# Kernel optimization log

Hardware: AMD Instinct MI355X
Metric: run time of the kernel (lower is better)

The kernel has to match this reference:

```python
import jax, jax.numpy as jnp
import numpy as np

B, L, N, C = 64, 12, 4096, 3
FD, HD, OUT = 32, 64, 12
TID, DIW, TD = 288, 7, 16
STEPS = 4
EMB = 10  # node embedding dim for learned adjacency


def setup_inputs() -> dict:
    key = jax.random.key(0)
    ks = jax.random.split(key, 16)
    g = lambda i, shape, s=0.05: jax.random.normal(ks[i], shape, dtype=jnp.float32) * s
    z = lambda n: jnp.zeros((n,), jnp.float32)
    return {
        "history_data": jax.random.uniform(ks[0], (B, L, N, C), dtype=jnp.float32),
        "future_data": jnp.zeros((B, L, N, 1), jnp.float32),
        "batch_seen": 0,
        "epoch": 0,
        "train": 1,
        "tid_emb": g(1, (TID, TD)),
        "diw_emb": g(2, (DIW, TD)),
        "t2f_w": g(3, (2 * TD, FD)), "t2f_b": z(FD),
        "enc_w1": g(4, (L * C, HD)), "enc_b1": z(HD),
        "enc_w2": g(5, (HD, FD)), "enc_b2": z(FD),
        "node_emb": g(6, (N, EMB), 1.0),
        "pde_w1": g(7, (FD, HD)), "pde_b1": z(HD),
        "pde_w2": g(8, (HD, FD)), "pde_b2": z(FD),
        "ss_win": g(9, (FD, FD)), "ss_wst": g(10, (FD, FD)), "ss_b": z(FD),
        "ss_wout": g(11, (FD, FD)), "ss_bout": z(FD),
        "dec_w1": g(12, (FD, HD)), "dec_b1": z(HD),
        "dec_w2": g(13, (HD, OUT)), "dec_b2": z(OUT),
        "pde_mix": jnp.array(0.5, jnp.float32),
    }


def reference(history_data, future_data, batch_seen, epoch, train,
              tid_emb, diw_emb, t2f_w, t2f_b,
              enc_w1, enc_b1, enc_w2, enc_b2,
              node_emb,
              pde_w1, pde_b1, pde_w2, pde_b2,
              ss_win, ss_wst, ss_b, ss_wout, ss_bout,
              dec_w1, dec_b1, dec_w2, dec_b2, pde_mix):
    # --- encoder: per-node MLP over flattened (L, C) history ---
    x = history_data[..., :C]                                    # [B,L,N,C]
    x = jnp.transpose(x, (0, 2, 1, 3)).reshape(B, N, L * C)      # [B,N,L*C]
    field = jnp.maximum(x @ enc_w1 + enc_b1, 0.0) @ enc_w2 + enc_b2  # [B,N,FD]

    # --- temporal field bias from last-step tid/diw ---
    tid_idx = jnp.clip((history_data[:, -1, :, 1] * TID).astype(jnp.int32), 0, TID - 1)
    diw_idx = jnp.clip((history_data[:, -1, :, 2] * DIW).astype(jnp.int32), 0, DIW - 1)
    temp = jnp.concatenate([tid_emb[tid_idx], diw_emb[diw_idx]], axis=-1)  # [B,N,2*TD]
    field = field + temp @ t2f_w + t2f_b

    # --- learned adjacency for graph Laplacian (L = I - A) ---
    A = jax.nn.softmax(jnp.maximum(node_emb @ node_emb.T, 0.0), axis=-1)  # [N,N]

    alpha = jax.nn.sigmoid(pde_mix)
    dt = 1.0 / STEPS
    state = jnp.zeros_like(field)
    for _ in range(STEPS):  # fixed small unroll over PDE steps
        L_F = jnp.einsum('nm,bmf->bnf', A, field) - field         # (A - I) F
        N_F = jnp.maximum(field @ pde_w1 + pde_b1, 0.0) @ pde_w2 + pde_b2
        fe = field + (alpha * L_F + (1.0 - alpha) * N_F) * dt
        state = jnp.tanh(fe @ ss_win + state @ ss_wst + ss_b)     # state-space update
        field = fe + state @ ss_wout + ss_bout

    # --- decoder: per-node MLP to output horizon ---
    pred = jnp.maximum(field @ dec_w1 + dec_b1, 0.0) @ dec_w2 + dec_b2  # [B,N,OUT]
    return jnp.transpose(pred, (0, 2, 1))[..., None]              # [B,OUT,N,1]
```

## Files before the change

kernel.cpp:

```cpp
#include <hip/hip_runtime.h>

#define BATCH 64
#define LHIST 12
#define NNODE 4096
#define CCH   3
#define FD    32
#define HD    64
#define OUTD  12
#define TIDN  288
#define DIWN  7
#define TDD   16
#define EMBD  10
#define MROWS 2048
#define KDIM  4096
#define MTOT  (BATCH * NNODE)

typedef __attribute__((ext_vector_type(8))) short bf16x8;
typedef __attribute__((ext_vector_type(4))) float f32x4;

union BF8U { bf16x8 v; unsigned short s[8]; };

__device__ __forceinline__ unsigned short f2b(float f) {
    union { float f; unsigned u; } v; v.f = f;
    unsigned r = v.u + 0x7fffu + ((v.u >> 16) & 1u);
    return (unsigned short)(r >> 16);
}

__device__ __forceinline__ float b2f(unsigned short u) {
    union { unsigned u; float f; } v; v.u = (unsigned)u << 16; return v.f;
}

__device__ __forceinline__ float fast_tanh(float x) {
    x = fminf(fmaxf(x, -15.f), 15.f);
    const float e = __expf(2.f * x);
    return (e - 1.f) / (e + 1.f);
}

__device__ __forceinline__ bf16x8 ldsfrag(const unsigned short* p) {
    return *(const bf16x8*)p;
}

__device__ __forceinline__ bf16x8 pack8(float4 a, float4 b) {
    BF8U u;
    u.s[0] = f2b(a.x); u.s[1] = f2b(a.y); u.s[2] = f2b(a.z); u.s[3] = f2b(a.w);
    u.s[4] = f2b(b.x); u.s[5] = f2b(b.y); u.s[6] = f2b(b.z); u.s[7] = f2b(b.w);
    return u.v;
}

__global__ __launch_bounds__(256) void build_A(const float* __restrict__ emb,
                                               unsigned short* __restrict__ A) {
    const int n = blockIdx.x;
    const int tid = threadIdx.x;
    __shared__ float sc[NNODE];
    __shared__ float red[256];
    float e[EMBD];
#pragma unroll
    for (int c = 0; c < EMBD; c++) e[c] = emb[(size_t)n * EMBD + c];
    float mx = 0.f;
    for (int m = tid; m < NNODE; m += 256) {
        float s = 0.f;
#pragma unroll
        for (int c = 0; c < EMBD; c++) s += e[c] * emb[(size_t)m * EMBD + c];
        s = fmaxf(s, 0.f);
        sc[m] = s;
        mx = fmaxf(mx, s);
    }
    red[tid] = mx;
    __syncthreads();
    for (int off = 128; off > 0; off >>= 1) {
        if (tid < off) red[tid] = fmaxf(red[tid], red[tid + off]);
        __syncthreads();
    }
    mx = red[0];
    __syncthreads();
    float sum = 0.f;
    for (int m = tid; m < NNODE; m += 256) {
        float v = expf(sc[m] - mx);
        sc[m] = v;
        sum += v;
    }
    red[tid] = sum;
    __syncthreads();
    for (int off = 128; off > 0; off >>= 1) {
        if (tid < off) red[tid] += red[tid + off];
        __syncthreads();
    }
    const float inv = 1.f / red[0];
    for (int m = tid; m < NNODE; m += 256)
        A[(size_t)n * NNODE + m] = f2b(sc[m] * inv);
}

__global__ __launch_bounds__(256, 2) void encoder(const float* __restrict__ hist,
                                                  const float* __restrict__ tid_emb,
                                                  const float* __restrict__ diw_emb,
                                                  const float* __restrict__ t2f_w,
                                                  const float* __restrict__ t2f_b,
                                                  const float* __restrict__ enc_w1,
                                                  const float* __restrict__ enc_b1,
                                                  const float* __restrict__ enc_w2,
                                                  const float* __restrict__ enc_b2,
                                                  float* __restrict__ field,
                                                  unsigned short* __restrict__ fT) {
    const int gid = blockIdx.x * 256 + threadIdx.x;
    const int b = gid >> 12;
    const int n = gid & (NNODE - 1);
    const float* hb = hist + ((size_t)b * LHIST * NNODE + n) * CCH;
    float x[LHIST * CCH];
#pragma unroll
    for (int l = 0; l < LHIST; l++) {
        x[l * 3 + 0] = hb[(size_t)l * NNODE * CCH + 0];
        x[l * 3 + 1] = hb[(size_t)l * NNODE * CCH + 1];
        x[l * 3 + 2] = hb[(size_t)l * NNODE * CCH + 2];
    }
    float f[FD];
#pragma unroll
    for (int o = 0; o < FD; o++) f[o] = enc_b2[o] + t2f_b[o];
    for (int j = 0; j < HD; j++) {
        float h = enc_b1[j];
#pragma unroll
        for (int k = 0; k < LHIST * CCH; k++) h += x[k] * enc_w1[k * HD + j];
        h = fmaxf(h, 0.f);
#pragma unroll
        for (int o = 0; o < FD; o++) f[o] += h * enc_w2[j * FD + o];
    }
    const int ti = min(max((int)(x[11 * 3 + 1] * 288.0f), 0), TIDN - 1);
    const int di = min(max((int)(x[11 * 3 + 2] * 7.0f), 0), DIWN - 1);
    for (int g = 0; g < TDD; g++) {
        const float tg = tid_emb[ti * TDD + g];
        const float dg = diw_emb[di * TDD + g];
#pragma unroll
        for (int o = 0; o < FD; o++)
            f[o] += tg * t2f_w[g * FD + o] + dg * t2f_w[(TDD + g) * FD + o];
    }
#pragma unroll
    for (int o4 = 0; o4 < FD / 4; o4++) {
        float4 v = {f[o4 * 4 + 0], f[o4 * 4 + 1], f[o4 * 4 + 2], f[o4 * 4 + 3]};
        *(float4*)&field[(size_t)gid * FD + o4 * 4] = v;
    }
#pragma unroll
    for (int o = 0; o < FD; o++)
        fT[(size_t)(b * FD + o) * NNODE + n] = f2b(f[o]);
}

#define TPAD 36
#define QHP  72
#define QFP  40
__global__ __launch_bounds__(256) void gemm_step(const unsigned short* __restrict__ X,
                                                 const unsigned short* __restrict__ Y,
                                                 float* __restrict__ field,
                                                 unsigned short* __restrict__ state,
                                                 unsigned short* __restrict__ fTo,
                                                 const float* __restrict__ pde_w1,
                                                 const float* __restrict__ pde_b1,
                                                 const float* __restrict__ pde_w2,
                                                 const float* __restrict__ pde_b2,
                                                 const float* __restrict__ ss_win,
                                                 const float* __restrict__ ss_wst,
                                                 const float* __restrict__ ss_b,
                                                 const float* __restrict__ ss_wout,
                                                 const float* __restrict__ ss_bout,
                                                 const float* __restrict__ pde_mix,
                                                 int first) {
    constexpr int K = KDIM;
    constexpr int BK = 32;
    __shared__ __align__(16) unsigned short SM0[512 * TPAD];
    __shared__ __align__(16) unsigned short W1T[HD * FD];
    __shared__ __align__(16) unsigned short W2T[FD * HD];
    __shared__ __align__(16) unsigned short WinT[FD * FD];
    __shared__ __align__(16) unsigned short WstT[FD * FD];
    __shared__ __align__(16) unsigned short WoutT[FD * FD];
    __shared__ __align__(16) unsigned short Hs[4 * 32 * QHP];
    __shared__ __align__(16) unsigned short Fs[4 * 32 * QFP];

    const int tid = threadIdx.x;
    const int wave = tid >> 6;
    const int lane = tid & 63;

    for (int i = tid; i < HD * FD; i += 256) W1T[(i & 63) * FD + (i >> 6)] = f2b(pde_w1[i]);
    for (int i = tid; i < HD * FD; i += 256) W2T[(i & 31) * HD + (i >> 5)] = f2b(pde_w2[i]);
    for (int i = tid; i < FD * FD; i += 256) {
        WinT [(i & 31) * FD + (i >> 5)] = f2b(ss_win[i]);
        WstT [(i & 31) * FD + (i >> 5)] = f2b(ss_wst[i]);
        WoutT[(i & 31) * FD + (i >> 5)] = f2b(ss_wout[i]);
    }

    const int l = blockIdx.x + 16 * blockIdx.y;
    const int xcd = l & 7;
    const int rem = l >> 3;
    const int by = xcd * 4 + (rem & 3);
    const int bx = rem >> 2;
    const int i0 = bx * 128;
    const int j0 = by * 128;
    const int b0 = i0 >> 5;

    const int wi = (wave >> 1) * 64;
    const int wj = (wave & 1) * 64;

    const int lrow = lane >> 2;
    const int gcol = (lane & 3) * 8;
    const int scol = ((lane & 3) ^ ((lane >> 3) & 3)) * 8;

    const unsigned short* Xg = X + (size_t)(i0 + wave * 32 + lrow) * K + gcol;
    const unsigned short* Yg = Y + (size_t)(j0 + wave * 32 + lrow) * K + gcol;
    unsigned short* Xs = SM0;
    unsigned short* Ys = SM0 + 8192;
    const int ld0 = (wave * 32 + lrow) * BK + scol;
    const int ld1 = (wave * 32 + 16 + lrow) * BK + scol;

    const f32x4 zero = {0.f, 0.f, 0.f, 0.f};
    f32x4 acc[4][4];
#pragma unroll
    for (int a = 0; a < 4; a++)
#pragma unroll
        for (int b = 0; b < 4; b++) acc[a][b] = zero;

    const int fr = lane & 15;
    const int q = lane >> 4;
    const int kq8 = (q ^ ((fr >> 1) & 3)) * 8;

#define GS_COMPUTE(P)                                                              \
    {                                                                              \
        bf16x8 fa[4], fb[4];                                                       \
        _Pragma("unroll") for (int t = 0; t < 4; t++)                              \
            fa[t] = *(const bf16x8*)&Xs[(P) * 4096 + (wi + t * 16 + fr) * BK + kq8]; \
        _Pragma("unroll") for (int t = 0; t < 4; t++)                              \
            fb[t] = *(const bf16x8*)&Ys[(P) * 4096 + (wj + t * 16 + fr) * BK + kq8]; \
        _Pragma("unroll") for (int mi = 0; mi < 4; mi++)                           \
            _Pragma("unroll") for (int ni = 0; ni < 4; ni++)                       \
                acc[mi][ni] = __builtin_amdgcn_mfma_f32_16x16x32_bf16(             \
                    fa[mi], fb[ni], acc[mi][ni], 0, 0, 0);                         \
    }

    uint4 ax0 = *(const uint4*)(Xg);
    uint4 ax1 = *(const uint4*)(Xg + 16 * K);
    uint4 ay0 = *(const uint4*)(Yg);
    uint4 ay1 = *(const uint4*)(Yg + 16 * K);
    uint4 bx0 = *(const uint4*)(Xg + BK);
    uint4 bx1 = *(const uint4*)(Xg + BK + 16 * K);
    uint4 by0 = *(const uint4*)(Yg + BK);
    uint4 by1 = *(const uint4*)(Yg + BK + 16 * K);
    *(uint4*)&Xs[ld0] = ax0; *(uint4*)&Xs[ld1] = ax1;
    *(uint4*)&Ys[ld0] = ay0; *(uint4*)&Ys[ld1] = ay1;
    __syncthreads();

    int p = 0;
    for (int kt = 0; kt < K; kt += 2 * BK) {
        if (kt + 2 * BK < K) {
            ax0 = *(const uint4*)(Xg + kt + 2 * BK);
            ax1 = *(const uint4*)(Xg + kt + 2 * BK + 16 * K);
            ay0 = *(const uint4*)(Yg + kt + 2 * BK);
            ay1 = *(const uint4*)(Yg + kt + 2 * BK + 16 * K);
        }
        GS_COMPUTE(p);
        {
            const int np = p ^ 1;
            *(uint4*)&Xs[np * 4096 + ld0] = bx0; *(uint4*)&Xs[np * 4096 + ld1] = bx1;
            *(uint4*)&Ys[np * 4096 + ld0] = by0; *(uint4*)&Ys[np * 4096 + ld1] = by1;
            __syncthreads();
        }
        if (kt + 3 * BK < K) {
            bx0 = *(const uint4*)(Xg + kt + 3 * BK);
            bx1 = *(const uint4*)(Xg + kt + 3 * BK + 16 * K);
            by0 = *(const uint4*)(Yg + kt + 3 * BK);
            by1 = *(const uint4*)(Yg + kt + 3 * BK + 16 * K);
        }
        GS_COMPUTE(p ^ 1);
        if (kt + 2 * BK < K) {
            *(uint4*)&Xs[p * 4096 + ld0] = ax0; *(uint4*)&Xs[p * 4096 + ld1] = ax1;
            *(uint4*)&Ys[p * 4096 + ld0] = ay0; *(uint4*)&Ys[p * 4096 + ld1] = ay1;
            __syncthreads();
        }
    }
#undef GS_COMPUTE

    __syncthreads();
    unsigned short* T = SM0;
    const int r0 = q * 4;
#pragma unroll
    for (int mi = 0; mi < 4; mi++) {
#pragma unroll
        for (int ni = 0; ni < 4; ni++) {
            const int R0 = i0 + wi + mi * 16 + r0;
            const int nl = wj + ni * 16 + fr;
            ushort4 pk = {f2b(acc[mi][ni][0]), f2b(acc[mi][ni][1]),
                          f2b(acc[mi][ni][2]), f2b(acc[mi][ni][3])};
            *(ushort4*)&T[((((R0 >> 5) & 3) << 7) + nl) * TPAD + (R0 & 31)] = pk;
        }
    }
    __syncthreads();

    const int ln = fr;
    const int kq = q * 8;
    unsigned short* Hw = &Hs[wave * 32 * QHP];
    unsigned short* Fw = &Fs[wave * 32 * QFP];
    const float alpha = 1.f / (1.f + __expf(-pde_mix[0]));
    const float dt = 0.25f;

    bf16x8 w1f[4], w2f[2][2], winf[2], wstf[2], woutf[2];
#pragma unroll
    for (int nj = 0; nj < 4; nj++) w1f[nj] = ldsfrag(&W1T[(nj * 16 + ln) * FD + kq]);
#pragma unroll
    for (int nf = 0; nf < 2; nf++) {
#pragma unroll
        for (int kk = 0; kk < 2; kk++)
            w2f[nf][kk] = ldsfrag(&W2T[(nf * 16 + ln) * HD + kk * 32 + kq]);
        winf[nf]  = ldsfrag(&WinT [(nf * 16 + ln) * FD + kq]);
        wstf[nf]  = ldsfrag(&WstT [(nf * 16 + ln) * FD + kq]);
        woutf[nf] = ldsfrag(&WoutT[(nf * 16 + ln) * FD + kq]);
    }
    float b1v[4], b2v[2], bsv[2], bov[2];
#pragma unroll
    for (int nj = 0; nj < 4; nj++) b1v[nj] = pde_b1[nj * 16 + ln];
#pragma unroll
    for (int nf = 0; nf < 2; nf++) {
        b2v[nf] = pde_b2[nf * 16 + ln];
        bsv[nf] = ss_b[nf * 16 + ln];
        bov[nf] = ss_bout[nf * 16 + ln];
    }

    for (int qtr = 0; qtr < 4; qtr++) {
        const int lb = wave * 128 + qtr * 32;
        const int bb = lb >> 7;
        const int nl0 = lb & 127;
        const int bg = b0 + bb;
        const int mwg = (bg << 12) + j0 + nl0;

        bf16x8 fA[2], stA[2];
#pragma unroll
        for (int mi = 0; mi < 2; mi++) {
            const float4* fp = (const float4*)&field[(size_t)(mwg + mi * 16 + ln) * FD + kq];
            fA[mi] = pack8(fp[0], fp[1]);
        }
        if (!first) {
#pragma unroll
            for (int mi = 0; mi < 2; mi++)
                stA[mi] = *(const bf16x8*)&state[(size_t)(mwg + mi * 16 + ln) * FD + kq];
        }

        f32x4 hc[2][4];
#pragma unroll
        for (int mi = 0; mi < 2; mi++)
#pragma unroll
            for (int nj = 0; nj < 4; nj++)
                hc[mi][nj] = __builtin_amdgcn_mfma_f32_16x16x32_bf16(fA[mi], w1f[nj], zero, 0, 0, 0);
#pragma unroll
        for (int mi = 0; mi < 2; mi++)
#pragma unroll
            for (int nj = 0; nj < 4; nj++)
#pragma unroll
                for (int r = 0; r < 4; r++)
                    Hw[(mi * 16 + r0 + r) * QHP + nj * 16 + ln] =
                        f2b(fmaxf(hc[mi][nj][r] + b1v[nj], 0.f));

        float fld[2][2][4], ctv[2][2][4];
#pragma unroll
        for (int mi = 0; mi < 2; mi++)
#pragma unroll
            for (int nf = 0; nf < 2; nf++)
#pragma unroll
                for (int r = 0; r < 4; r++) {
                    const size_t idx = (size_t)(mwg + mi * 16 + r0 + r) * FD + nf * 16 + ln;
                    fld[mi][nf][r] = field[idx];
                    ctv[mi][nf][r] = b2f(T[(lb + mi * 16 + r0 + r) * TPAD + nf * 16 + ln]);
                }

        bf16x8 hA[2][2];
#pragma unroll
        for (int mi = 0; mi < 2; mi++)
#pragma unroll
            for (int kk = 0; kk < 2; kk++)
                hA[mi][kk] = ldsfrag(&Hw[(mi * 16 + ln) * QHP + kk * 32 + kq]);
        f32x4 nc[2][2];
#pragma unroll
        for (int mi = 0; mi < 2; mi++)
#pragma unroll
            for (int nf = 0; nf < 2; nf++) {
                f32x4 a = __builtin_amdgcn_mfma_f32_16x16x32_bf16(hA[mi][0], w2f[nf][0], zero, 0, 0, 0);
                nc[mi][nf] = __builtin_amdgcn_mfma_f32_16x16x32_bf16(hA[mi][1], w2f[nf][1], a, 0, 0, 0);
            }

        float fe[2][2][4];
#pragma unroll
        for (int mi = 0; mi < 2; mi++)
#pragma unroll
            for (int nf = 0; nf < 2; nf++)
#pragma unroll
                for (int r = 0; r < 4; r++) {
                    const float nfv = nc[mi][nf][r] + b2v[nf];
                    const float fv = fld[mi][nf][r];
                    fe[mi][nf][r] = fv + (alpha * (ctv[mi][nf][r] - fv) + (1.f - alpha) * nfv) * dt;
                    Fw[(mi * 16 + r0 + r) * QFP + nf * 16 + ln] = f2b(fe[mi][nf][r]);
                }

        bf16x8 feA[2];
#pragma unroll
        for (int mi = 0; mi < 2; mi++) feA[mi] = ldsfrag(&Fw[(mi * 16 + ln) * QFP + kq]);
        f32x4 sc_[2][2];
#pragma unroll
        for (int mi = 0; mi < 2; mi++)
#pragma unroll
            for (int nf = 0; nf < 2; nf++) {
                f32x4 a = __builtin_amdgcn_mfma_f32_16x16x32_bf16(feA[mi], winf[nf], zero, 0, 0, 0);
                if (!first)
                    a = __builtin_amdgcn_mfma_f32_16x16x32_bf16(stA[mi], wstf[nf], a, 0, 0, 0);
                sc_[mi][nf] = a;
            }
        float sval[2][2][4];
#pragma unroll
        for (int mi = 0; mi < 2; mi++)
#pragma unroll
            for (int nf = 0; nf < 2; nf++)
#pragma unroll
                for (int r = 0; r < 4; r++)
                    sval[mi][nf][r] = fast_tanh(sc_[mi][nf][r] + bsv[nf]);
#pragma unroll
        for (int mi = 0; mi < 2; mi++)
#pragma unroll
            for (int nf = 0; nf < 2; nf++)
#pragma unroll
                for (int r = 0; r < 4; r++)
                    Fw[(mi * 16 + r0 + r) * QFP + nf * 16 + ln] = f2b(sval[mi][nf][r]);

        bf16x8 SA[2];
#pragma unroll
        for (int mi = 0; mi < 2; mi++) SA[mi] = ldsfrag(&Fw[(mi * 16 + ln) * QFP + kq]);
#pragma unroll
        for (int mi = 0; mi < 2; mi++) {
#pragma unroll
            for (int nf = 0; nf < 2; nf++) {
                f32x4 oc = __builtin_amdgcn_mfma_f32_16x16x32_bf16(SA[mi], woutf[nf], zero, 0, 0, 0);
                float fnew[4];
#pragma unroll
                for (int r = 0; r < 4; r++) {
                    fnew[r] = fe[mi][nf][r] + oc[r] + bov[nf];
                    const size_t idx = (size_t)(mwg + mi * 16 + r0 + r) * FD + nf * 16 + ln;
                    field[idx] = fnew[r];
                    state[idx] = f2b(sval[mi][nf][r]);
                }
                ushort4 pk = {f2b(fnew[0]), f2b(fnew[1]), f2b(fnew[2]), f2b(fnew[3])};
                const size_t fta = (size_t)(bg * FD + nf * 16 + ln) * NNODE
                                 + j0 + nl0 + mi * 16 + r0;
                *(ushort4*)&fTo[fta] = pk;
            }
        }
    }
}

__global__ __launch_bounds__(256) void gemm_bt(const unsigned short* __restrict__ X,
                                               const unsigned short* __restrict__ Y,
                                               unsigned short* __restrict__ Cp) {
    constexpr int K = KDIM;
    constexpr int KS = KDIM / 2;
    constexpr int BK = 32;
    __shared__ __align__(16) unsigned short Xs[2 * 4096];
    __shared__ __align__(16) unsigned short Ys[2 * 4096];
    const int tid = threadIdx.x;
    const int wave = tid >> 6;
    const int lane = tid & 63;

    const int l = blockIdx.x + 16 * blockIdx.y;
    const int xcd = l & 7;
    const int rem = l >> 3;
    const int by = xcd * 4 + (rem & 3);
    const int bx = rem >> 2;
    const int i0 = bx * 128;
    const int j0 = by * 128;
    const int k0 = blockIdx.z * KS;
    unsigned short* C = Cp + (size_t)blockIdx.z * MTOT * FD;

    const int wi = (wave >> 1) * 64;
    const int wj = (wave & 1) * 64;

    const int lrow = lane >> 2;
    const int gcol = (lane & 3) * 8;
    const int scol = ((lane & 3) ^ ((lane >> 3) & 3)) * 8;

    const unsigned short* Xg = X + (size_t)(i0 + wave * 32 + lrow) * K + k0 + gcol;
    const unsigned short* Yg = Y + (size_t)(j0 + wave * 32 + lrow) * K + k0 + gcol;
    const int ld0 = (wave * 32 + lrow) * BK + scol;
    const int ld1 = (wave * 32 + 16 + lrow) * BK + scol;

    const f32x4 zero = {0.f, 0.f, 0.f, 0.f};
    f32x4 acc[4][4];
#pragma unroll
    for (int a = 0; a < 4; a++)
#pragma unroll
        for (int b = 0; b < 4; b++) acc[a][b] = zero;

    const int fr = lane & 15;
    const int q = lane >> 4;
    const int kq8 = (q ^ ((fr >> 1) & 3)) * 8;

#define GB_COMPUTE(P)                                                              \
    {                                                                              \
        bf16x8 fa[4], fb[4];                                                       \
        _Pragma("unroll") for (int t = 0; t < 4; t++)                              \
            fa[t] = *(const bf16x8*)&Xs[(P) * 4096 + (wi + t * 16 + fr) * BK + kq8]; \
        _Pragma("unroll") for (int t = 0; t < 4; t++)                              \
            fb[t] = *(const bf16x8*)&Ys[(P) * 4096 + (wj + t * 16 + fr) * BK + kq8]; \
        _Pragma("unroll") for (int mi = 0; mi < 4; mi++)                           \
            _Pragma("unroll") for (int ni = 0; ni < 4; ni++)                       \
                acc[mi][ni] = __builtin_amdgcn_mfma_f32_16x16x32_bf16(             \
                    fa[mi], fb[ni], acc[mi][ni], 0, 0, 0);                         \
    }

    uint4 ax0 = *(const uint4*)(Xg);
    uint4 ax1 = *(const uint4*)(Xg + 16 * K);
    uint4 ay0 = *(const uint4*)(Yg);
    uint4 ay1 = *(const uint4*)(Yg + 16 * K);
    uint4 bx0 = *(const uint4*)(Xg + BK);
    uint4 bx1 = *(const uint4*)(Xg + BK + 16 * K);
    uint4 by0 = *(const uint4*)(Yg + BK);
    uint4 by1 = *(const uint4*)(Yg + BK + 16 * K);
    *(uint4*)&Xs[ld0] = ax0; *(uint4*)&Xs[ld1] = ax1;
    *(uint4*)&Ys[ld0] = ay0; *(uint4*)&Ys[ld1] = ay1;
    __syncthreads();

    int p = 0;
    for (int kt = 0; kt < KS; kt += 2 * BK) {
        if (kt + 2 * BK < KS) {
            ax0 = *(const uint4*)(Xg + kt + 2 * BK);
            ax1 = *(const uint4*)(Xg + kt + 2 * BK + 16 * K);
            ay0 = *(const uint4*)(Yg + kt + 2 * BK);
            ay1 = *(const uint4*)(Yg + kt + 2 * BK + 16 * K);
        }
        GB_COMPUTE(p);
        {
            const int np = p ^ 1;
            *(uint4*)&Xs[np * 4096 + ld0] = bx0; *(uint4*)&Xs[np * 4096 + ld1] = bx1;
            *(uint4*)&Ys[np * 4096 + ld0] = by0; *(uint4*)&Ys[np * 4096 + ld1] = by1;
            __syncthreads();
        }
        if (kt + 3 * BK < KS) {
            bx0 = *(const uint4*)(Xg + kt + 3 * BK);
            bx1 = *(const uint4*)(Xg + kt + 3 * BK + 16 * K);
            by0 = *(const uint4*)(Yg + kt + 3 * BK);
            by1 = *(const uint4*)(Yg + kt + 3 * BK + 16 * K);
        }
        GB_COMPUTE(p ^ 1);
        if (kt + 2 * BK < KS) {
            *(uint4*)&Xs[p * 4096 + ld0] = ax0; *(uint4*)&Xs[p * 4096 + ld1] = ax1;
            *(uint4*)&Ys[p * 4096 + ld0] = ay0; *(uint4*)&Ys[p * 4096 + ld1] = ay1;
            __syncthreads();
        }
    }
#undef GB_COMPUTE

    const int r0 = q * 4;
#pragma unroll
    for (int mi = 0; mi < 4; mi++) {
#pragma unroll
        for (int ni = 0; ni < 4; ni++) {
            const int R0 = i0 + wi + mi * 16 + r0;
            const int col = j0 + wj + ni * 16 + fr;
            const size_t addr = ((size_t)(R0 >> 5) * NNODE + col) * FD + (R0 & 31);
            ushort4 pk = {f2b(acc[mi][ni][0]), f2b(acc[mi][ni][1]),
                          f2b(acc[mi][ni][2]), f2b(acc[mi][ni][3])};
            *(ushort4*)&C[addr] = pk;
        }
    }
}

#define HPAD 72
#define FPAD 40
__global__ __launch_bounds__(256, 2) void step_mfma(const unsigned short* __restrict__ Ct0,
                                                    const unsigned short* __restrict__ Ct1,
                                                    float* __restrict__ field,
                                                    unsigned short* __restrict__ state,
                                                    const float* __restrict__ pde_w1,
                                                    const float* __restrict__ pde_b1,
                                                    const float* __restrict__ pde_w2,
                                                    const float* __restrict__ pde_b2,
                                                    const float* __restrict__ ss_win,
                                                    const float* __restrict__ ss_wst,
                                                    const float* __restrict__ ss_b,
                                                    const float* __restrict__ ss_wout,
                                                    const float* __restrict__ ss_bout,
                                                    const float* __restrict__ pde_mix,
                                                    const float* __restrict__ dec_w1,
                                                    const float* __restrict__ dec_b1,
                                                    const float* __restrict__ dec_w2,
                                                    const float* __restrict__ dec_b2,
                                                    float* __restrict__ out) {
    __shared__ __align__(16) unsigned short W1T[HD * FD];
    __shared__ __align__(16) unsigned short W2T[FD * HD];
    __shared__ __align__(16) unsigned short WinT[FD * FD];
    __shared__ __align__(16) unsigned short WstT[FD * FD];
    __shared__ __align__(16) unsigned short WoutT[FD * FD];
    __shared__ __align__(16) unsigned short Wd1T[HD * FD];
    __shared__ __align__(16) unsigned short Wd2T[16 * HD];
    __shared__ __align__(16) unsigned short Hs[4 * 64 * HPAD];
    __shared__ __align__(16) unsigned short Fs[4 * 64 * FPAD];

    const int tid = threadIdx.x;
    for (int i = tid; i < HD * FD; i += 256) W1T[(i & 63) * FD + (i >> 6)] = f2b(pde_w1[i]);
    for (int i = tid; i < HD * FD; i += 256) W2T[(i & 31) * HD + (i >> 5)] = f2b(pde_w2[i]);
    for (int i = tid; i < FD * FD; i += 256) {
        WinT [(i & 31) * FD + (i >> 5)] = f2b(ss_win[i]);
        WstT [(i & 31) * FD + (i >> 5)] = f2b(ss_wst[i]);
        WoutT[(i & 31) * FD + (i >> 5)] = f2b(ss_wout[i]);
    }
    for (int i = tid; i < HD * FD; i += 256)
        Wd1T[(i & 63) * FD + (i >> 6)] = f2b(dec_w1[i]);
    for (int i = tid; i < 16 * HD; i += 256) {
        const int o = i >> 6, j = i & 63;
        Wd2T[i] = (o < OUTD) ? f2b(dec_w2[j * OUTD + o]) : (unsigned short)0;
    }
    __syncthreads();

    const int wv = tid >> 6;
    const int lane = tid & 63;
    const int ln = lane & 15;
    const int q = lane >> 4;
    const int kq = q * 8;
    const int r0 = q * 4;
    const int mw = blockIdx.x * 256 + wv * 64;
    const int b = mw >> 12;
    const int n0 = mw & (NNODE - 1);
    unsigned short* Hw = &Hs[wv * 64 * HPAD];
    unsigned short* Fw = &Fs[wv * 64 * FPAD];

    const float alpha = 1.f / (1.f + __expf(-pde_mix[0]));
    const float dt = 0.25f;

    bf16x8 w1f[4], w2f[2][2], winf[2], wstf[2], woutf[2];
#pragma unroll
    for (int nj = 0; nj < 4; nj++) w1f[nj] = ldsfrag(&W1T[(nj * 16 + ln) * FD + kq]);
#pragma unroll
    for (int nf = 0; nf < 2; nf++) {
#pragma unroll
        for (int kk = 0; kk < 2; kk++)
            w2f[nf][kk] = ldsfrag(&W2T[(nf * 16 + ln) * HD + kk * 32 + kq]);
        winf[nf]  = ldsfrag(&WinT [(nf * 16 + ln) * FD + kq]);
        wstf[nf]  = ldsfrag(&WstT [(nf * 16 + ln) * FD + kq]);
        woutf[nf] = ldsfrag(&WoutT[(nf * 16 + ln) * FD + kq]);
    }

    float b1v[4], b2v[2], bsv[2], bov[2];
#pragma unroll
    for (int nj = 0; nj < 4; nj++) b1v[nj] = pde_b1[nj * 16 + ln];
#pragma unroll
    for (int nf = 0; nf < 2; nf++) {
        b2v[nf] = pde_b2[nf * 16 + ln];
        bsv[nf] = ss_b[nf * 16 + ln];
        bov[nf] = ss_bout[nf * 16 + ln];
    }

    bf16x8 fA[4], stA[4];
#pragma unroll
    for (int mi = 0; mi < 4; mi++) {
        const float4* fp = (const float4*)&field[(size_t)(mw + mi * 16 + ln) * FD + kq];
        fA[mi] = pack8(fp[0], fp[1]);
    }
#pragma unroll
    for (int mi = 0; mi < 4; mi++)
        stA[mi] = *(const bf16x8*)&state[(size_t)(mw + mi * 16 + ln) * FD + kq];

    const f32x4 zero = {0.f, 0.f, 0.f, 0.f};

    f32x4 hc[4][4];
#pragma unroll
    for (int mi = 0; mi < 4; mi++)
#pragma unroll
        for (int nj = 0; nj < 4; nj++)
            hc[mi][nj] = __builtin_amdgcn_mfma_f32_16x16x32_bf16(fA[mi], w1f[nj], zero, 0, 0, 0);
#pragma unroll
    for (int mi = 0; mi < 4; mi++)
#pragma unroll
        for (int nj = 0; nj < 4; nj++)
#pragma unroll
            for (int r = 0; r < 4; r++)
                Hw[(mi * 16 + r0 + r) * HPAD + nj * 16 + ln] =
                    f2b(fmaxf(hc[mi][nj][r] + b1v[nj], 0.f));

    float fld[4][2][4], ctv[4][2][4];
#pragma unroll
    for (int mi = 0; mi < 4; mi++)
#pragma unroll
        for (int nf = 0; nf < 2; nf++)
#pragma unroll
            for (int r = 0; r < 4; r++) {
                const size_t idx = (size_t)(mw + mi * 16 + r0 + r) * FD + nf * 16 + ln;
                fld[mi][nf][r] = field[idx];
                ctv[mi][nf][r] = b2f(Ct0[idx]) + b2f(Ct1[idx]);
            }

    bf16x8 hA[4][2];
#pragma unroll
    for (int mi = 0; mi < 4; mi++)
#pragma unroll
        for (int kk = 0; kk < 2; kk++)
            hA[mi][kk] = ldsfrag(&Hw[(mi * 16 + ln) * HPAD + kk * 32 + kq]);
    f32x4 nc[4][2];
#pragma unroll
    for (int mi = 0; mi < 4; mi++)
#pragma unroll
        for (int nf = 0; nf < 2; nf++) {
            f32x4 a = __builtin_amdgcn_mfma_f32_16x16x32_bf16(hA[mi][0], w2f[nf][0], zero, 0, 0, 0);
            nc[mi][nf] = __builtin_amdgcn_mfma_f32_16x16x32_bf16(hA[mi][1], w2f[nf][1], a, 0, 0, 0);
        }

    float fe[4][2][4];
#pragma unroll
    for (int mi = 0; mi < 4; mi++)
#pragma unroll
        for (int nf = 0; nf < 2; nf++)
#pragma unroll
            for (int r = 0; r < 4; r++) {
                const float nfv = nc[mi][nf][r] + b2v[nf];
                const float fv = fld[mi][nf][r];
                fe[mi][nf][r] = fv + (alpha * (ctv[mi][nf][r] - fv) + (1.f - alpha) * nfv) * dt;
                Fw[(mi * 16 + r0 + r) * FPAD + nf * 16 + ln] = f2b(fe[mi][nf][r]);
            }

    bf16x8 feA[4];
#pragma unroll
    for (int mi = 0; mi < 4; mi++) feA[mi] = ldsfrag(&Fw[(mi * 16 + ln) * FPAD + kq]);
    f32x4 sc_[4][2];
#pragma unroll
    for (int mi = 0; mi < 4; mi++)
#pragma unroll
        for (int nf = 0; nf < 2; nf++) {
            f32x4 a = __builtin_amdgcn_mfma_f32_16x16x32_bf16(feA[mi], winf[nf], zero, 0, 0, 0);
            a = __builtin_amdgcn_mfma_f32_16x16x32_bf16(stA[mi], wstf[nf], a, 0, 0, 0);
            sc_[mi][nf] = a;
        }
    float sval[4][2][4];
#pragma unroll
    for (int mi = 0; mi < 4; mi++)
#pragma unroll
        for (int nf = 0; nf < 2; nf++)
#pragma unroll
            for (int r = 0; r < 4; r++)
                sval[mi][nf][r] = fast_tanh(sc_[mi][nf][r] + bsv[nf]);
#pragma unroll
    for (int mi = 0; mi < 4; mi++)
#pragma unroll
        for (int nf = 0; nf < 2; nf++)
#pragma unroll
            for (int r = 0; r < 4; r++)
                Fw[(mi * 16 + r0 + r) * FPAD + nf * 16 + ln] = f2b(sval[mi][nf][r]);

    bf16x8 SA[4];
#pragma unroll
    for (int mi = 0; mi < 4; mi++) SA[mi] = ldsfrag(&Fw[(mi * 16 + ln) * FPAD + kq]);
    float fnew[4][2][4];
#pragma unroll
    for (int mi = 0; mi < 4; mi++)
#pragma unroll
        for (int nf = 0; nf < 2; nf++) {
            f32x4 oc = __builtin_amdgcn_mfma_f32_16x16x32_bf16(SA[mi], woutf[nf], zero, 0, 0, 0);
#pragma unroll
            for (int r = 0; r < 4; r++)
                fnew[mi][nf][r] = fe[mi][nf][r] + oc[r] + bov[nf];
        }

    bf16x8 wd1f[4], wd2f[2];
#pragma unroll
    for (int nj = 0; nj < 4; nj++) wd1f[nj] = ldsfrag(&Wd1T[(nj * 16 + ln) * FD + kq]);
#pragma unroll
    for (int kk = 0; kk < 2; kk++) wd2f[kk] = ldsfrag(&Wd2T[ln * HD + kk * 32 + kq]);
    float db1v[4];
#pragma unroll
    for (int nj = 0; nj < 4; nj++) db1v[nj] = dec_b1[nj * 16 + ln];
    const float db2v = (ln < OUTD) ? dec_b2[ln] : 0.f;

#pragma unroll
    for (int mi = 0; mi < 4; mi++)
#pragma unroll
        for (int nf = 0; nf < 2; nf++)
#pragma unroll
            for (int r = 0; r < 4; r++)
                Fw[(mi * 16 + r0 + r) * FPAD + nf * 16 + ln] = f2b(fnew[mi][nf][r]);
    bf16x8 fnA[4];
#pragma unroll
    for (int mi = 0; mi < 4; mi++) fnA[mi] = ldsfrag(&Fw[(mi * 16 + ln) * FPAD + kq]);

    f32x4 h2[4][4];
#pragma unroll
    for (int mi = 0; mi < 4; mi++)
#pragma unroll
        for (int nj = 0; nj < 4; nj++)
            h2[mi][nj] = __builtin_amdgcn_mfma_f32_16x16x32_bf16(fnA[mi], wd1f[nj], zero, 0, 0, 0);
#pragma unroll
    for (int mi = 0; mi < 4; mi++)
#pragma unroll
        for (int nj = 0; nj < 4; nj++)
#pragma unroll
            for (int r = 0; r < 4; r++)
                Hw[(mi * 16 + r0 + r) * HPAD + nj * 16 + ln] =
                    f2b(fmaxf(h2[mi][nj][r] + db1v[nj], 0.f));
    bf16x8 h2A[4][2];
#pragma unroll
    for (int mi = 0; mi < 4; mi++)
#pragma unroll
        for (int kk = 0; kk < 2; kk++)
            h2A[mi][kk] = ldsfrag(&Hw[(mi * 16 + ln) * HPAD + kk * 32 + kq]);
#pragma unroll
    for (int mi = 0; mi < 4; mi++) {
        f32x4 a = __builtin_amdgcn_mfma_f32_16x16x32_bf16(h2A[mi][0], wd2f[0], zero, 0, 0, 0);
        a = __builtin_amdgcn_mfma_f32_16x16x32_bf16(h2A[mi][1], wd2f[1], a, 0, 0, 0);
        if (ln < OUTD) {
            float4 v = {a[0] + db2v, a[1] + db2v, a[2] + db2v, a[3] + db2v};
            *(float4*)&out[(size_t)(b * OUTD + ln) * NNODE + n0 + mi * 16 + r0] = v;
        }
    }
}

extern "C" void kernel_launch(void* const* d_in, const int* in_sizes, int n_in,
                              void* d_out, int out_size, void* d_ws, size_t ws_size,
                              hipStream_t stream) {
    (void)in_sizes; (void)n_in; (void)out_size; (void)ws_size;
    const float* hist    = (const float*)d_in[0];
    const float* tid_emb = (const float*)d_in[5];
    const float* diw_emb = (const float*)d_in[6];
    const float* t2f_w   = (const float*)d_in[7];
    const float* t2f_b   = (const float*)d_in[8];
    const float* enc_w1  = (const float*)d_in[9];
    const float* enc_b1  = (const float*)d_in[10];
    const float* enc_w2  = (const float*)d_in[11];
    const float* enc_b2  = (const float*)d_in[12];
    const float* node_emb= (const float*)d_in[13];
    const float* pde_w1  = (const float*)d_in[14];
    const float* pde_b1  = (const float*)d_in[15];
    const float* pde_w2  = (const float*)d_in[16];
    const float* pde_b2  = (const float*)d_in[17];
    const float* ss_win  = (const float*)d_in[18];
    const float* ss_wst  = (const float*)d_in[19];
    const float* ss_b    = (const float*)d_in[20];
    const float* ss_wout = (const float*)d_in[21];
    const float* ss_bout = (const float*)d_in[22];
    const float* dec_w1  = (const float*)d_in[23];
    const float* dec_b1  = (const float*)d_in[24];
    const float* dec_w2  = (const float*)d_in[25];
    const float* dec_b2  = (const float*)d_in[26];
    const float* pde_mix = (const float*)d_in[27];

    char* w = (char*)d_ws;
    unsigned short* A_bf = (unsigned short*)w;  w += (size_t)KDIM * KDIM * 2;
    unsigned short* fTa  = (unsigned short*)w;  w += (size_t)MROWS * KDIM * 2;
    unsigned short* fTb  = (unsigned short*)w;  w += (size_t)MROWS * KDIM * 2;
    float* field = (float*)w;                   w += (size_t)MTOT * FD * 4;
    unsigned short* state = (unsigned short*)w; w += (size_t)MTOT * FD * 2;
    unsigned short* Cp    = (unsigned short*)w; w += (size_t)2 * MTOT * FD * 2;

    build_A<<<NNODE, 256, 0, stream>>>(node_emb, A_bf);
    encoder<<<(BATCH * NNODE) / 256, 256, 0, stream>>>(hist, tid_emb, diw_emb, t2f_w,
                                                       t2f_b, enc_w1, enc_b1, enc_w2,
                                                       enc_b2, field, fTa);
    unsigned short* fts[4] = {fTa, fTb, fTa, fTb};
    for (int s = 0; s < 3; s++) {
        gemm_step<<<dim3(16, 32), 256, 0, stream>>>(
            fts[s], A_bf, field, state, fts[s + 1], pde_w1, pde_b1, pde_w2, pde_b2,
            ss_win, ss_wst, ss_b, ss_wout, ss_bout, pde_mix, s == 0 ? 1 : 0);
    }
    gemm_bt<<<dim3(16, 32, 2), 256, 0, stream>>>(fts[3], A_bf, Cp);
    step_mfma<<<MTOT / 256, 256, 0, stream>>>(
        Cp, Cp + (size_t)MTOT * FD, field, state, pde_w1, pde_b1, pde_w2, pde_b2,
        ss_win, ss_wst, ss_b, ss_wout, ss_bout, pde_mix,
        dec_w1, dec_b1, dec_w2, dec_b2, (float*)d_out);
}
```

Before: 683.5 us.

## Stream GEMM tiles directly global-to-LDS with async loads in graph GEMMs

Both A·F GEMM kernels now use global_load_lds (direct global to shared-memory DMA) instead of staging through registers and then storing to LDS. The XOR swizzle moves from the LDS write address to the global read column, so LDS rows keep the same swizzled layout. The loop becomes a simple double buffer with one barrier per K tile. This is meant to free VGPRs and remove LDS store instructions, at the cost of relying on the barrier to also wait for the async loads and a shallower prefetch distance than the previous two-stage register pipeline.

```diff
diff --git a/kernel.cpp b/kernel.cpp
--- a/kernel.cpp
+++ b/kernel.cpp
@@ -34,6 +34,11 @@
     x = fminf(fmaxf(x, -15.f), 15.f);
     const float e = __expf(2.f * x);
     return (e - 1.f) / (e + 1.f);
+}
+
+__device__ __forceinline__ void gl2lds16(const void* g, void* l) {
+    __builtin_amdgcn_global_load_lds((__attribute__((address_space(1))) void*)(void*)g,
+                                     (__attribute__((address_space(3))) void*)l, 16, 0, 0);
 }
 
 __device__ __forceinline__ bf16x8 ldsfrag(const unsigned short* p) {
@@ -197,15 +202,16 @@
     const int wj = (wave & 1) * 64;
 
     const int lrow = lane >> 2;
-    const int gcol = (lane & 3) * 8;
-    const int scol = ((lane & 3) ^ ((lane >> 3) & 3)) * 8;
+    const int gcol = ((lane & 3) ^ ((lane >> 3) & 3)) * 8;
 
     const unsigned short* Xg = X + (size_t)(i0 + wave * 32 + lrow) * K + gcol;
     const unsigned short* Yg = Y + (size_t)(j0 + wave * 32 + lrow) * K + gcol;
-    unsigned short* Xs = SM0;
-    unsigned short* Ys = SM0 + 8192;
-    const int ld0 = (wave * 32 + lrow) * BK + scol;
-    const int ld1 = (wave * 32 + 16 + lrow) * BK + scol;
+    unsigned short* XsB = SM0;
+    unsigned short* YsB = SM0 + 8192;
+    unsigned short* Xd0 = XsB + (wave * 32) * BK;
+    unsigned short* Xd1 = XsB + (wave * 32 + 16) * BK;
+    unsigned short* Yd0 = YsB + (wave * 32) * BK;
+    unsigned short* Yd1 = YsB + (wave * 32 + 16) * BK;
 
     const f32x4 zero = {0.f, 0.f, 0.f, 0.f};
     f32x4 acc[4][4];
@@ -218,62 +224,37 @@
     const int q = lane >> 4;
     const int kq8 = (q ^ ((fr >> 1) & 3)) * 8;
 
-#define GS_COMPUTE(P)                                                              \
-    {                                                                              \
-        bf16x8 fa[4], fb[4];                                                       \
-        _Pragma("unroll") for (int t = 0; t < 4; t++)                              \
-            fa[t] = *(const bf16x8*)&Xs[(P) * 4096 + (wi + t * 16 + fr) * BK + kq8]; \
-        _Pragma("unroll") for (int t = 0; t < 4; t++)                              \
-            fb[t] = *(const bf16x8*)&Ys[(P) * 4096 + (wj + t * 16 + fr) * BK + kq8]; \
-        _Pragma("unroll") for (int mi = 0; mi < 4; mi++)                           \
-            _Pragma("unroll") for (int ni = 0; ni < 4; ni++)                       \
-                acc[mi][ni] = __builtin_amdgcn_mfma_f32_16x16x32_bf16(             \
-                    fa[mi], fb[ni], acc[mi][ni], 0, 0, 0);                         \
-    }
-
-    uint4 ax0 = *(const uint4*)(Xg);
-    uint4 ax1 = *(const uint4*)(Xg + 16 * K);
-    uint4 ay0 = *(const uint4*)(Yg);
-    uint4 ay1 = *(const uint4*)(Yg + 16 * K);
-    uint4 bx0 = *(const uint4*)(Xg + BK);
-    uint4 bx1 = *(const uint4*)(Xg + BK + 16 * K);
-    uint4 by0 = *(const uint4*)(Yg + BK);
-    uint4 by1 = *(const uint4*)(Yg + BK + 16 * K);
-    *(uint4*)&Xs[ld0] = ax0; *(uint4*)&Xs[ld1] = ax1;
-    *(uint4*)&Ys[ld0] = ay0; *(uint4*)&Ys[ld1] = ay1;
+#define GS_ISSUE(P, KT)                                        \
+    gl2lds16(Xg + (KT), Xd0 + (P) * 4096);                     \
+    gl2lds16(Xg + (KT) + 16 * K, Xd1 + (P) * 4096);            \
+    gl2lds16(Yg + (KT), Yd0 + (P) * 4096);                     \
+    gl2lds16(Yg + (KT) + 16 * K, Yd1 + (P) * 4096);
+
+#define GS_COMPUTE(P)                                                                 \
+    {                                                                                 \
+        bf16x8 fa[4], fb[4];                                                          \
+        _Pragma("unroll") for (int t = 0; t < 4; t++)                                 \
+            fa[t] = *(const bf16x8*)&XsB[(P) * 4096 + (wi + t * 16 + fr) * BK + kq8]; \
+        _Pragma("unroll") for (int t = 0; t < 4; t++)                                 \
+            fb[t] = *(const bf16x8*)&YsB[(P) * 4096 + (wj + t * 16 + fr) * BK + kq8]; \
+        _Pragma("unroll") for (int mi = 0; mi < 4; mi++)                              \
+            _Pragma("unroll") for (int ni = 0; ni < 4; ni++)                          \
+                acc[mi][ni] = __builtin_amdgcn_mfma_f32_16x16x32_bf16(                \
+                    fa[mi], fb[ni], acc[mi][ni], 0, 0, 0);                            \
+    }
+
+    GS_ISSUE(0, 0);
     __syncthreads();
-
     int p = 0;
-    for (int kt = 0; kt < K; kt += 2 * BK) {
-        if (kt + 2 * BK < K) {
-            ax0 = *(const uint4*)(Xg + kt + 2 * BK);
-            ax1 = *(const uint4*)(Xg + kt + 2 * BK + 16 * K);
-            ay0 = *(const uint4*)(Yg + kt + 2 * BK);
-            ay1 = *(const uint4*)(Yg + kt + 2 * BK + 16 * K);
-        }
+    for (int kt = 0; kt < K; kt += BK) {
+        if (kt + BK < K) { GS_ISSUE(p ^ 1, kt + BK); }
         GS_COMPUTE(p);
-        {
-            const int np = p ^ 1;
-            *(uint4*)&Xs[np * 4096 + ld0] = bx0; *(uint4*)&Xs[np * 4096 + ld1] = bx1;
-            *(uint4*)&Ys[np * 4096 + ld0] = by0; *(uint4*)&Ys[np * 4096 + ld1] = by1;
-            __syncthreads();
-        }
-        if (kt + 3 * BK < K) {
-            bx0 = *(const uint4*)(Xg + kt + 3 * BK);
-            bx1 = *(const uint4*)(Xg + kt + 3 * BK + 16 * K);
-            by0 = *(const uint4*)(Yg + kt + 3 * BK);
-            by1 = *(const uint4*)(Yg + kt + 3 * BK + 16 * K);
-        }
-        GS_COMPUTE(p ^ 1);
-        if (kt + 2 * BK < K) {
-            *(uint4*)&Xs[p * 4096 + ld0] = ax0; *(uint4*)&Xs[p * 4096 + ld1] = ax1;
-            *(uint4*)&Ys[p * 4096 + ld0] = ay0; *(uint4*)&Ys[p * 4096 + ld1] = ay1;
-            __syncthreads();
-        }
+        __syncthreads();
+        p ^= 1;
     }
 #undef GS_COMPUTE
-
-    __syncthreads();
+#undef GS_ISSUE
+
     unsigned short* T = SM0;
     const int r0 = q * 4;
 #pragma unroll
@@ -472,13 +453,14 @@
     const int wj = (wave & 1) * 64;
 
     const int lrow = lane >> 2;
-    const int gcol = (lane & 3) * 8;
-    const int scol = ((lane & 3) ^ ((lane >> 3) & 3)) * 8;
+    const int gcol = ((lane & 3) ^ ((lane >> 3) & 3)) * 8;
 
     const unsigned short* Xg = X + (size_t)(i0 + wave * 32 + lrow) * K + k0 + gcol;
     const unsigned short* Yg = Y + (size_t)(j0 + wave * 32 + lrow) * K + k0 + gcol;
-    const int ld0 = (wave * 32 + lrow) * BK + scol;
-    const int ld1 = (wave * 32 + 16 + lrow) * BK + scol;
+    unsigned short* Xd0 = Xs + (wave * 32) * BK;
+    unsigned short* Xd1 = Xs + (wave * 32 + 16) * BK;
+    unsigned short* Yd0 = Ys + (wave * 32) * BK;
+    unsigned short* Yd1 = Ys + (wave * 32 + 16) * BK;
 
     const f32x4 zero = {0.f, 0.f, 0.f, 0.f};
     f32x4 acc[4][4];
@@ -491,60 +473,36 @@
     const int q = lane >> 4;
     const int kq8 = (q ^ ((fr >> 1) & 3)) * 8;
 
-#define GB_COMPUTE(P)                                                              \
-    {                                                                              \
-        bf16x8 fa[4], fb[4];                                                       \
-        _Pragma("unroll") for (int t = 0; t < 4; t++)                              \
+#define GB_ISSUE(P, KT)                                        \
+    gl2lds16(Xg + (KT), Xd0 + (P) * 4096);                     \
+    gl2lds16(Xg + (KT) + 16 * K, Xd1 + (P) * 4096);            \
+    gl2lds16(Yg + (KT), Yd0 + (P) * 4096);                     \
+    gl2lds16(Yg + (KT) + 16 * K, Yd1 + (P) * 4096);
+
+#define GB_COMPUTE(P)                                                                \
+    {                                                                                \
+        bf16x8 fa[4], fb[4];                                                         \
+        _Pragma("unroll") for (int t = 0; t < 4; t++)                                \
             fa[t] = *(const bf16x8*)&Xs[(P) * 4096 + (wi + t * 16 + fr) * BK + kq8]; \
-        _Pragma("unroll") for (int t = 0; t < 4; t++)                              \
+        _Pragma("unroll") for (int t = 0; t < 4; t++)                                \
             fb[t] = *(const bf16x8*)&Ys[(P) * 4096 + (wj + t * 16 + fr) * BK + kq8]; \
-        _Pragma("unroll") for (int mi = 0; mi < 4; mi++)                           \
-            _Pragma("unroll") for (int ni = 0; ni < 4; ni++)                       \
-                acc[mi][ni] = __builtin_amdgcn_mfma_f32_16x16x32_bf16(             \
-                    fa[mi], fb[ni], acc[mi][ni], 0, 0, 0);                         \
-    }
-
-    uint4 ax0 = *(const uint4*)(Xg);
-    uint4 ax1 = *(const uint4*)(Xg + 16 * K);
-    uint4 ay0 = *(const uint4*)(Yg);
-    uint4 ay1 = *(const uint4*)(Yg + 16 * K);
-    uint4 bx0 = *(const uint4*)(Xg + BK);
-    uint4 bx1 = *(const uint4*)(Xg + BK + 16 * K);
-    uint4 by0 = *(const uint4*)(Yg + BK);
-    uint4 by1 = *(const uint4*)(Yg + BK + 16 * K);
-    *(uint4*)&Xs[ld0] = ax0; *(uint4*)&Xs[ld1] = ax1;
-    *(uint4*)&Ys[ld0] = ay0; *(uint4*)&Ys[ld1] = ay1;
+        _Pragma("unroll") for (int mi = 0; mi < 4; mi++)                             \
+            _Pragma("unroll") for (int ni = 0; ni < 4; ni++)                         \
+                acc[mi][ni] = __builtin_amdgcn_mfma_f32_16x16x32_bf16(               \
+                    fa[mi], fb[ni], acc[mi][ni], 0, 0, 0);                           \
+    }
+
+    GB_ISSUE(0, 0);
     __syncthreads();
-
     int p = 0;
-    for (int kt = 0; kt < KS; kt += 2 * BK) {
-        if (kt + 2 * BK < KS) {
-            ax0 = *(const uint4*)(Xg + kt + 2 * BK);
-            ax1 = *(const uint4*)(Xg + kt + 2 * BK + 16 * K);
-            ay0 = *(const uint4*)(Yg + kt + 2 * BK);
-            ay1 = *(const uint4*)(Yg + kt + 2 * BK + 16 * K);
-        }
+    for (int kt = 0; kt < KS; kt += BK) {
+        if (kt + BK < KS) { GB_ISSUE(p ^ 1, kt + BK); }
         GB_COMPUTE(p);
-        {
-            const int np = p ^ 1;
-            *(uint4*)&Xs[np * 4096 + ld0] = bx0; *(uint4*)&Xs[np * 4096 + ld1] = bx1;
-            *(uint4*)&Ys[np * 4096 + ld0] = by0; *(uint4*)&Ys[np * 4096 + ld1] = by1;
-            __syncthreads();
-        }
-        if (kt + 3 * BK < KS) {
-            bx0 = *(const uint4*)(Xg + kt + 3 * BK);
-            bx1 = *(const uint4*)(Xg + kt + 3 * BK + 16 * K);
-            by0 = *(const uint4*)(Yg + kt + 3 * BK);
-            by1 = *(const uint4*)(Yg + kt + 3 * BK + 16 * K);
-        }
-        GB_COMPUTE(p ^ 1);
-        if (kt + 2 * BK < KS) {
-            *(uint4*)&Xs[p * 4096 + ld0] = ax0; *(uint4*)&Xs[p * 4096 + ld1] = ax1;
-            *(uint4*)&Ys[p * 4096 + ld0] = ay0; *(uint4*)&Ys[p * 4096 + ld1] = ay1;
-            __syncthreads();
-        }
+        __syncthreads();
+        p ^= 1;
     }
 #undef GB_COMPUTE
+#undef GB_ISSUE
 
     const int r0 = q * 4;
 #pragma unroll
```

New measurement: 700.6 us. 1.03x slower.
